# Kernel optimization log

Measured on AMD Instinct MI355X. Metric: run time of the kernel, lower is better.

## Reference

```python
import jax, jax.numpy as jnp
import numpy as np

LN2 = float(np.log(2.0))
N_ATOMS = 100_000
N_PAIRS = 2_000_000
F = 64     # number_of_atom_features
R = 16     # number_of_radial_basis_functions
N_RES = 3


def setup_inputs() -> dict:
    key = jax.random.key(0)
    ks = jax.random.split(key, 16)
    s = 0.05
    inp = {
        "pair_indices": jax.random.randint(ks[0], (2, N_PAIRS), 0, N_ATOMS, dtype=jnp.int32),
        "f_ij": jax.random.normal(ks[1], (N_PAIRS, 1, R), dtype=jnp.float32),
        "d_ij": jax.random.uniform(ks[2], (N_PAIRS, 1), dtype=jnp.float32),
        "atomic_embedding": jax.random.normal(ks[3], (N_ATOMS, F), dtype=jnp.float32),
        # AttentionMask parameter G: [F, R]
        "G": jax.random.normal(ks[4], (F, R), dtype=jnp.float32),
        # interaction_i / interaction_j linear layers (stored as [in, out])
        "Wi": jax.random.normal(ks[5], (F, F), dtype=jnp.float32) * s,
        "bi": jnp.zeros((F,), dtype=jnp.float32),
        "Wj": jax.random.normal(ks[6], (F, F), dtype=jnp.float32) * s,
        "bj": jnp.zeros((F,), dtype=jnp.float32),
        # residual blocks, stacked over N_RES
        "res_W1": jax.random.normal(ks[7], (N_RES, F, F), dtype=jnp.float32) * s,
        "res_b1": jnp.zeros((N_RES, F), dtype=jnp.float32),
        "res_W2": jax.random.normal(ks[8], (N_RES, F, F), dtype=jnp.float32) * s,
        "res_b2": jnp.zeros((N_RES, F), dtype=jnp.float32),
        # process_v linear
        "Wv": jax.random.normal(ks[9], (F, F), dtype=jnp.float32) * s,
        "bv": jnp.zeros((F,), dtype=jnp.float32),
    }
    return inp


def reference(pair_indices, f_ij, d_ij, atomic_embedding,
              G, Wi, bi, Wj, bj, res_W1, res_b1, res_W2, res_b2, Wv, bv):
    idx_i, idx_j = pair_indices[0], pair_indices[1]
    f = f_ij.squeeze(1)                                  # [P, R]

    # ShiftedSoftplus on node embeddings
    x = jax.nn.softplus(atomic_embedding) - LN2          # [N, F]

    x_i_prime = jax.nn.softplus(x @ Wi + bi)             # [N, F]
    x_j_prime = jax.nn.softplus(x[idx_j] @ Wj + bj)      # [P, F] (gather)
    f_prime = f @ G.T                                    # [P, F] attention mask

    msg = x_j_prime * f_prime                            # [P, F]
    summed = jax.ops.segment_sum(msg, idx_i, num_segments=atomic_embedding.shape[0])

    v = x_i_prime + summed                               # [N, F]
    for l in range(res_W1.shape[0]):
        h = jax.nn.softplus(v @ res_W1[l] + res_b1[l])
        v = v + (h @ res_W2[l] + res_b2[l])
    return jax.nn.softplus(v) @ Wv + bv
```

## Files before the change

### kernel.cpp

```cpp
#include <hip/hip_runtime.h>
#include <math.h>

#define FDIM 64
#define RDIM 16
#define LN2F 0.69314718055994530942f
#define LTS 68
#define NBINR 14336
#define NCHUNK 64

typedef __bf16 bf8_t __attribute__((ext_vector_type(8)));
typedef float  f4_t  __attribute__((ext_vector_type(4)));
typedef _Float16 h2_t __attribute__((ext_vector_type(2)));

__device__ __forceinline__ float sp(float x) {
    return fmaxf(x, 0.0f) + __logf(1.0f + __expf(-fabsf(x)));
}

__device__ __forceinline__ float fdot2f(h2_t a, h2_t b, float c) {
#if __has_builtin(__builtin_amdgcn_fdot2)
    return __builtin_amdgcn_fdot2(a, b, c, false);
#else
    return c + (float)a[0] * (float)b[0] + (float)a[1] * (float)b[1];
#endif
}

__device__ __forceinline__ void cvt_store16(_Float16* dst, float4 A, float4 B,
                                            float4 C4, float4 D)
{
    h2_t hv[8];
    hv[0] = h2_t{(_Float16)A.x,  (_Float16)A.y};
    hv[1] = h2_t{(_Float16)A.z,  (_Float16)A.w};
    hv[2] = h2_t{(_Float16)B.x,  (_Float16)B.y};
    hv[3] = h2_t{(_Float16)B.z,  (_Float16)B.w};
    hv[4] = h2_t{(_Float16)C4.x, (_Float16)C4.y};
    hv[5] = h2_t{(_Float16)C4.z, (_Float16)C4.w};
    hv[6] = h2_t{(_Float16)D.x,  (_Float16)D.y};
    hv[7] = h2_t{(_Float16)D.z,  (_Float16)D.w};
    *(uint4*)dst       = *(const uint4*)&hv[0];
    *(uint4*)(dst + 8) = *(const uint4*)&hv[4];
}

__global__ __launch_bounds__(256) void k_prep(
    const float* s0, const float* s1, const float* s2, const float* s3,
    const float* s4, const float* s5, const float* s6, const float* s7,
    const float* s8, __bf16* __restrict__ dst)
{
    const float* srcs[9] = {s0, s1, s2, s3, s4, s5, s6, s7, s8};
    const float* W = srcs[blockIdx.x];
    __bf16* d = dst + (size_t)blockIdx.x * 4096;
    for (int slot = threadIdx.x; slot < 512; slot += 256) {
        int f = slot >> 6, l = slot & 63;
        int kt = f >> 2, nt = f & 3;
        int row0 = kt * 32 + (l >> 4) * 8;
        int col = nt * 16 + (l & 15);
#pragma unroll
        for (int j = 0; j < 8; ++j)
            d[slot * 8 + j] = (__bf16)W[(row0 + j) * FDIM + col];
    }
}

__global__ __launch_bounds__(256) void k_hist2(
    const int* __restrict__ idx_i, int* __restrict__ Cmat,
    int P, int N, int nRange)
{
    __shared__ int h[NBINR];
    const int chunk = blockIdx.x / nRange;
    const int range = blockIdx.x % nRange;
    const int lo = range * NBINR;
    const int nb = min(NBINR, N - lo);
    for (int u = threadIdx.x; u < NBINR; u += 256) h[u] = 0;
    __syncthreads();

    const int chunkSz = (P + NCHUNK - 1) / NCHUNK;
    const int cs = chunk * chunkSz;
    const int ce = min(P, cs + chunkSz);
    int p = cs + threadIdx.x;
    for (; p + 768 < ce; p += 1024) {
        int i0 = idx_i[p];
        int i1 = idx_i[p + 256];
        int i2 = idx_i[p + 512];
        int i3 = idx_i[p + 768];
        unsigned u0 = (unsigned)(i0 - lo);
        unsigned u1 = (unsigned)(i1 - lo);
        unsigned u2 = (unsigned)(i2 - lo);
        unsigned u3 = (unsigned)(i3 - lo);
        if (u0 < (unsigned)nb) atomicAdd(&h[u0], 1);
        if (u1 < (unsigned)nb) atomicAdd(&h[u1], 1);
        if (u2 < (unsigned)nb) atomicAdd(&h[u2], 1);
        if (u3 < (unsigned)nb) atomicAdd(&h[u3], 1);
    }
    for (; p < ce; p += 256) {
        unsigned u = (unsigned)(idx_i[p] - lo);
        if (u < (unsigned)nb) atomicAdd(&h[u], 1);
    }
    __syncthreads();
    for (int u = threadIdx.x; u < nb; u += 256)
        Cmat[(size_t)chunk * N + lo + u] = h[u];
}

__global__ __launch_bounds__(256) void k_scanR(
    int* __restrict__ Cmat, int* __restrict__ tot, int N)
{
    const int bA = blockIdx.x * 512 + threadIdx.x;
    const int bB = bA + 256;
    const bool okA = bA < N, okB = bB < N;
    int runA = 0, runB = 0;
    for (int c = 0; c < NCHUNK; ++c) {
        const size_t base = (size_t)c * N;
        if (okA) { int val = Cmat[base + bA]; Cmat[base + bA] = runA; runA += val; }
        if (okB) { int val = Cmat[base + bB]; Cmat[base + bB] = runB; runB += val; }
    }
    if (okA) tot[bA] = runA;
    if (okB) tot[bB] = runB;
}

__device__ __forceinline__ void tile_in(float* T, const float* __restrict__ src,
                                        int a0, int rows, int lane)
{
#pragma unroll 4
    for (int i = 0; i < 16; ++i) {
        int r = i * 4 + (lane >> 4);
        int col = (lane & 15) * 4;
        float4 val = make_float4(0.f, 0.f, 0.f, 0.f);
        if (r < rows) val = *(const float4*)&src[(size_t)(a0 + r) * FDIM + col];
        *(float4*)&T[r * LTS + col] = val;
    }
}

__device__ __forceinline__ void build_a(const float* T, int lane, bool actLn2,
                                        bf8_t (&aF)[4][2])
{
    const int l15 = lane & 15, quad = lane >> 4;
#pragma unroll
    for (int mt = 0; mt < 4; ++mt) {
#pragma unroll
        for (int kt = 0; kt < 2; ++kt) {
            const float* rp = &T[(mt * 16 + l15) * LTS + kt * 32 + quad * 8];
            float4 u0 = *(const float4*)rp;
            float4 u1 = *(const float4*)(rp + 4);
            float e[8] = {u0.x, u0.y, u0.z, u0.w, u1.x, u1.y, u1.z, u1.w};
            bf8_t f;
#pragma unroll
            for (int j = 0; j < 8; ++j) {
                float t = actLn2 ? (sp(e[j]) - LN2F) : e[j];
                f[j] = (__bf16)t;
            }
            aF[mt][kt] = f;
        }
    }
}

__global__ __launch_bounds__(256) void k_atoms(
    const float* __restrict__ emb, const __bf16* __restrict__ wf,
    const float* __restrict__ bi, const float* __restrict__ bj,
    float* __restrict__ v, _Float16* __restrict__ y16, int N)
{
    __shared__ float tile[4][64 * LTS];
    const int lane = threadIdx.x & 63;
    const int wv = threadIdx.x >> 6;
    float* T = tile[wv];
    const int l15 = lane & 15, quad = lane >> 4;

    const bf8_t* wiF = (const bf8_t*)wf;
    const bf8_t* wjF = (const bf8_t*)(wf + 4096);
    bf8_t wi[2][4], wj[2][4];
#pragma unroll
    for (int kt = 0; kt < 2; ++kt)
#pragma unroll
        for (int nt = 0; nt < 4; ++nt) {
            wi[kt][nt] = wiF[(kt * 4 + nt) * 64 + lane];
            wj[kt][nt] = wjF[(kt * 4 + nt) * 64 + lane];
        }
    float biv[4], bjv[4];
#pragma unroll
    for (int nt = 0; nt < 4; ++nt) {
        biv[nt] = bi[nt * 16 + l15];
        bjv[nt] = bj[nt * 16 + l15];
    }

    const int nTiles = (N + 63) >> 6;
    for (int t = blockIdx.x * 4 + wv; t < nTiles; t += gridDim.x * 4) {
        const int a0 = t << 6;
        const int rows = min(64, N - a0);
        tile_in(T, emb, a0, rows, lane);
        bf8_t aF[4][2];
        build_a(T, lane, true, aF);
#pragma unroll
        for (int mt = 0; mt < 4; ++mt)
#pragma unroll
            for (int nt = 0; nt < 4; ++nt) {
                f4_t acc = {biv[nt], biv[nt], biv[nt], biv[nt]};
                acc = __builtin_amdgcn_mfma_f32_16x16x32_bf16(aF[mt][0], wi[0][nt], acc, 0, 0, 0);
                acc = __builtin_amdgcn_mfma_f32_16x16x32_bf16(aF[mt][1], wi[1][nt], acc, 0, 0, 0);
#pragma unroll
                for (int reg = 0; reg < 4; ++reg) {
                    int r = mt * 16 + quad * 4 + reg;
                    if (r < rows) v[(size_t)(a0 + r) * FDIM + nt * 16 + l15] = sp(acc[reg]);
                }
            }
#pragma unroll
        for (int mt = 0; mt < 4; ++mt)
#pragma unroll
            for (int nt = 0; nt < 4; ++nt) {
                f4_t acc = {bjv[nt], bjv[nt], bjv[nt], bjv[nt]};
                acc = __builtin_amdgcn_mfma_f32_16x16x32_bf16(aF[mt][0], wj[0][nt], acc, 0, 0, 0);
                acc = __builtin_amdgcn_mfma_f32_16x16x32_bf16(aF[mt][1], wj[1][nt], acc, 0, 0, 0);
#pragma unroll
                for (int reg = 0; reg < 4; ++reg) {
                    int r = mt * 16 + quad * 4 + reg;
                    if (r < rows)
                        y16[(size_t)(a0 + r) * FDIM + nt * 16 + l15] = (_Float16)sp(acc[reg]);
                }
            }
    }
}

__global__ __launch_bounds__(256) void k_post(
    const __bf16* __restrict__ wf,
    const float* __restrict__ rb1, const float* __restrict__ rb2,
    const float* __restrict__ bv,
    float* __restrict__ v, int N)
{
    __shared__ float tile[4][64 * LTS];
    const int lane = threadIdx.x & 63;
    const int wv = threadIdx.x >> 6;
    float* T = tile[wv];
    const int l15 = lane & 15, quad = lane >> 4;

    float b1v[3][4], b2v[3][4], bvv[4];
#pragma unroll
    for (int l = 0; l < 3; ++l)
#pragma unroll
        for (int nt = 0; nt < 4; ++nt) {
            b1v[l][nt] = rb1[l * FDIM + nt * 16 + l15];
            b2v[l][nt] = rb2[l * FDIM + nt * 16 + l15];
        }
#pragma unroll
    for (int nt = 0; nt < 4; ++nt) bvv[nt] = bv[nt * 16 + l15];

    const int nTiles = (N + 63) >> 6;
    for (int t = blockIdx.x * 4 + wv; t < nTiles; t += gridDim.x * 4) {
        const int a0 = t << 6;
        const int rows = min(64, N - a0);
        tile_in(T, v, a0, rows, lane);
        float vC[16][4];
#pragma unroll
        for (int mt = 0; mt < 4; ++mt)
#pragma unroll
            for (int nt = 0; nt < 4; ++nt)
#pragma unroll
                for (int reg = 0; reg < 4; ++reg)
                    vC[mt * 4 + nt][reg] =
                        T[(mt * 16 + quad * 4 + reg) * LTS + nt * 16 + l15];

        for (int l = 0; l < 3; ++l) {
            const bf8_t* w1f = (const bf8_t*)(wf + (size_t)(2 * l) * 4096);
            const bf8_t* w2f = (const bf8_t*)(wf + (size_t)(2 * l + 1) * 4096);
            bf8_t aF[4][2];
            build_a(T, lane, false, aF);
#pragma unroll
            for (int mt = 0; mt < 4; ++mt)
#pragma unroll
                for (int nt = 0; nt < 4; ++nt) {
                    f4_t acc = {b1v[l][nt], b1v[l][nt], b1v[l][nt], b1v[l][nt]};
                    acc = __builtin_amdgcn_mfma_f32_16x16x32_bf16(aF[mt][0], w1f[(0 * 4 + nt) * 64 + lane], acc, 0, 0, 0);
                    acc = __builtin_amdgcn_mfma_f32_16x16x32_bf16(aF[mt][1], w1f[(1 * 4 + nt) * 64 + lane], acc, 0, 0, 0);
#pragma unroll
                    for (int reg = 0; reg < 4; ++reg)
                        T[(mt * 16 + quad * 4 + reg) * LTS + nt * 16 + l15] = sp(acc[reg]);
                }
            bf8_t hF[4][2];
            build_a(T, lane, false, hF);
#pragma unroll
            for (int mt = 0; mt < 4; ++mt)
#pragma unroll
                for (int nt = 0; nt < 4; ++nt) {
                    f4_t acc = {b2v[l][nt], b2v[l][nt], b2v[l][nt], b2v[l][nt]};
                    acc = __builtin_amdgcn_mfma_f32_16x16x32_bf16(hF[mt][0], w2f[(0 * 4 + nt) * 64 + lane], acc, 0, 0, 0);
                    acc = __builtin_amdgcn_mfma_f32_16x16x32_bf16(hF[mt][1], w2f[(1 * 4 + nt) * 64 + lane], acc, 0, 0, 0);
#pragma unroll
                    for (int reg = 0; reg < 4; ++reg)
                        vC[mt * 4 + nt][reg] += acc[reg];
                }
            if (l < 2) {
#pragma unroll
                for (int mt = 0; mt < 4; ++mt)
#pragma unroll
                    for (int nt = 0; nt < 4; ++nt)
#pragma unroll
                        for (int reg = 0; reg < 4; ++reg)
                            T[(mt * 16 + quad * 4 + reg) * LTS + nt * 16 + l15] =
                                vC[mt * 4 + nt][reg];
            }
        }
#pragma unroll
        for (int mt = 0; mt < 4; ++mt)
#pragma unroll
            for (int nt = 0; nt < 4; ++nt)
#pragma unroll
                for (int reg = 0; reg < 4; ++reg)
                    T[(mt * 16 + quad * 4 + reg) * LTS + nt * 16 + l15] =
                        sp(vC[mt * 4 + nt][reg]);
        bf8_t fF[4][2];
        build_a(T, lane, false, fF);
        const bf8_t* wvf = (const bf8_t*)(wf + (size_t)6 * 4096);
#pragma unroll
        for (int mt = 0; mt < 4; ++mt)
#pragma unroll
            for (int nt = 0; nt < 4; ++nt) {
                f4_t acc = {bvv[nt], bvv[nt], bvv[nt], bvv[nt]};
                acc = __builtin_amdgcn_mfma_f32_16x16x32_bf16(fF[mt][0], wvf[(0 * 4 + nt) * 64 + lane], acc, 0, 0, 0);
                acc = __builtin_amdgcn_mfma_f32_16x16x32_bf16(fF[mt][1], wvf[(1 * 4 + nt) * 64 + lane], acc, 0, 0, 0);
#pragma unroll
                for (int reg = 0; reg < 4; ++reg) {
                    int r = mt * 16 + quad * 4 + reg;
                    if (r < rows) v[(size_t)(a0 + r) * FDIM + nt * 16 + l15] = acc[reg];
                }
            }
    }
}

__global__ __launch_bounds__(256) void k_scan_a(
    const int* __restrict__ cnt, int* __restrict__ part, int N)
{
    __shared__ int red[256];
    int b = blockIdx.x, t = threadIdx.x;
    int base = b * 1024 + t * 4;
    int s = 0;
#pragma unroll
    for (int i = 0; i < 4; ++i) { int a = base + i; if (a < N) s += cnt[a]; }
    red[t] = s; __syncthreads();
    for (int off = 128; off > 0; off >>= 1) {
        if (t < off) red[t] += red[t + off];
        __syncthreads();
    }
    if (t == 0) part[b] = red[0];
}

__global__ __launch_bounds__(256) void k_scan_b(int* __restrict__ part, int nPart)
{
    __shared__ int lds[256];
    int t = threadIdx.x;
    int base = t * 4;
    int v[4]; int s = 0;
#pragma unroll
    for (int i = 0; i < 4; ++i) { v[i] = (base + i < nPart) ? part[base + i] : 0; s += v[i]; }
    lds[t] = s; __syncthreads();
    int run = s;
    for (int off = 1; off < 256; off <<= 1) {
        int x = (t >= off) ? lds[t - off] : 0;
        __syncthreads();
        lds[t] += x;
        __syncthreads();
    }
    int excl = lds[t] - run;
#pragma unroll
    for (int i = 0; i < 4; ++i) { if (base + i < nPart) { part[base + i] = excl; excl += v[i]; } }
}

__global__ __launch_bounds__(256) void k_scan_c(
    const int* __restrict__ cnt, const int* __restrict__ part,
    int* __restrict__ start, int N, int P)
{
    __shared__ int lds[256];
    int b = blockIdx.x, t = threadIdx.x;
    int base = b * 1024 + t * 4;
    int v[4]; int s = 0;
#pragma unroll
    for (int i = 0; i < 4; ++i) { int a = base + i; v[i] = (a < N) ? cnt[a] : 0; s += v[i]; }
    lds[t] = s; __syncthreads();
    int run = s;
    for (int off = 1; off < 256; off <<= 1) {
        int x = (t >= off) ? lds[t - off] : 0;
        __syncthreads();
        lds[t] += x;
        __syncthreads();
    }
    int pre = part[b] + (lds[t] - run);
#pragma unroll
    for (int i = 0; i < 4; ++i) {
        int a = base + i;
        if (a < N) { start[a] = pre; pre += v[i]; }
    }
    if (b == 0 && t == 0) start[N] = P;
}

__global__ __launch_bounds__(256) void k_scatter2(
    const int* __restrict__ pidx, const int* __restrict__ Cmat,
    const int* __restrict__ start, int* __restrict__ sortedJ,
    int* __restrict__ invPos, int P, int N, int nRange)
{
    __shared__ int cur[NBINR];
    const int chunk = blockIdx.x / nRange;
    const int range = blockIdx.x % nRange;
    const int lo = range * NBINR;
    const int nb = min(NBINR, N - lo);
    for (int u = threadIdx.x; u < nb; u += 256)
        cur[u] = start[lo + u] + Cmat[(size_t)chunk * N + lo + u];
    __syncthreads();

    const int chunkSz = (P + NCHUNK - 1) / NCHUNK;
    const int cs = chunk * chunkSz;
    const int ce = min(P, cs + chunkSz);
    int p = cs + threadIdx.x;
    for (; p + 768 < ce; p += 1024) {
        int i0 = pidx[p];
        int i1 = pidx[p + 256];
        int i2 = pidx[p + 512];
        int i3 = pidx[p + 768];
        int j0 = pidx[P + p];
        int j1 = pidx[P + p + 256];
        int j2 = pidx[P + p + 512];
        int j3 = pidx[P + p + 768];
        unsigned u0 = (unsigned)(i0 - lo);
        unsigned u1 = (unsigned)(i1 - lo);
        unsigned u2 = (unsigned)(i2 - lo);
        unsigned u3 = (unsigned)(i3 - lo);
        if (u0 < (unsigned)nb) { int pos = atomicAdd(&cur[u0], 1); sortedJ[pos] = j0; invPos[p] = pos; }
        if (u1 < (unsigned)nb) { int pos = atomicAdd(&cur[u1], 1); sortedJ[pos] = j1; invPos[p + 256] = pos; }
        if (u2 < (unsigned)nb) { int pos = atomicAdd(&cur[u2], 1); sortedJ[pos] = j2; invPos[p + 512] = pos; }
        if (u3 < (unsigned)nb) { int pos = atomicAdd(&cur[u3], 1); sortedJ[pos] = j3; invPos[p + 768] = pos; }
    }
    for (; p < ce; p += 256) {
        int i = pidx[p];
        unsigned u = (unsigned)(i - lo);
        if (u < (unsigned)nb) {
            int j = pidx[P + p];
            int pos = atomicAdd(&cur[u], 1);
            sortedJ[pos] = j;
            invPos[p] = pos;
        }
    }
}

__global__ __launch_bounds__(256) void k_gatherF2(
    const float* __restrict__ f_ij, const int* __restrict__ invPos,
    _Float16* __restrict__ sortedF, int P)
{
    int t = blockIdx.x * blockDim.x + threadIdx.x;
    int n = gridDim.x * blockDim.x;
    int p = t;
    for (; p + 3 * n < P; p += 4 * n) {
        int q0 = invPos[p];
        int q1 = invPos[p + n];
        int q2 = invPos[p + 2 * n];
        int q3 = invPos[p + 3 * n];
        const float4* f0 = (const float4*)(f_ij + (size_t)p * RDIM);
        const float4* f1 = (const float4*)(f_ij + (size_t)(p + n) * RDIM);
        const float4* f2 = (const float4*)(f_ij + (size_t)(p + 2 * n) * RDIM);
        const float4* f3 = (const float4*)(f_ij + (size_t)(p + 3 * n) * RDIM);
        float4 a0 = f0[0], b0 = f0[1], c0 = f0[2], d0 = f0[3];
        float4 a1 = f1[0], b1 = f1[1], c1 = f1[2], d1 = f1[3];
        float4 a2 = f2[0], b2 = f2[1], c2 = f2[2], d2 = f2[3];
        float4 a3 = f3[0], b3 = f3[1], c3 = f3[2], d3 = f3[3];
        cvt_store16(sortedF + (size_t)q0 * 16, a0, b0, c0, d0);
        cvt_store16(sortedF + (size_t)q1 * 16, a1, b1, c1, d1);
        cvt_store16(sortedF + (size_t)q2 * 16, a2, b2, c2, d2);
        cvt_store16(sortedF + (size_t)q3 * 16, a3, b3, c3, d3);
    }
    for (; p < P; p += n) {
        int q = invPos[p];
        const float4* fp = (const float4*)(f_ij + (size_t)p * RDIM);
        float4 A = fp[0], B = fp[1], C4 = fp[2], D = fp[3];
        cvt_store16(sortedF + (size_t)q * 16, A, B, C4, D);
    }
}

__global__ __launch_bounds__(256) void k_seg(
    const int* __restrict__ sortedJ, const _Float16* __restrict__ sortedF,
    const int* __restrict__ start, const float* __restrict__ G,
    const _Float16* __restrict__ y16, float* __restrict__ v, int N)
{
    const int c = threadIdx.x & 63;
    const int w = __builtin_amdgcn_readfirstlane((blockIdx.x << 2) | (threadIdx.x >> 6));
    const int nw = gridDim.x << 2;

    h2_t g2[8];
    {
        const float4* gp = (const float4*)(G + c * RDIM);
        float4 g0 = gp[0], g1 = gp[1], g2v = gp[2], g3 = gp[3];
        g2[0] = h2_t{(_Float16)g0.x, (_Float16)g0.y};
        g2[1] = h2_t{(_Float16)g0.z, (_Float16)g0.w};
        g2[2] = h2_t{(_Float16)g1.x, (_Float16)g1.y};
        g2[3] = h2_t{(_Float16)g1.z, (_Float16)g1.w};
        g2[4] = h2_t{(_Float16)g2v.x, (_Float16)g2v.y};
        g2[5] = h2_t{(_Float16)g2v.z, (_Float16)g2v.w};
        g2[6] = h2_t{(_Float16)g3.x, (_Float16)g3.y};
        g2[7] = h2_t{(_Float16)g3.z, (_Float16)g3.w};
    }

    for (int a = w; a < N; a += nw) {
        const int s = __builtin_amdgcn_readfirstlane(start[a]);
        const int e = __builtin_amdgcn_readfirstlane(start[a + 1]);
        float vold = v[(size_t)a * FDIM + c];
        float acc0 = 0.f, acc1 = 0.f, acc2 = 0.f, acc3 = 0.f;

        for (int base = s; base < e; base += 64) {
            const int nn = (e - base < 64) ? (e - base) : 64;
            const int li = (c < nn) ? c : (nn - 1);
            const int jkv = sortedJ[base + li];

            int k = 0;
            for (; k + 8 <= nn; k += 8) {
                int jj[8];
#pragma unroll
                for (int u = 0; u < 8; ++u)
                    jj[u] = __builtin_amdgcn_readlane(jkv, k + u);
                float yv[8];
#pragma unroll
                for (int u = 0; u < 8; ++u)
                    yv[u] = (float)y16[(size_t)jj[u] * FDIM + c];
                const h2_t* f2 = (const h2_t*)(sortedF + (size_t)(base + k) * 16);
#pragma unroll
                for (int u = 0; u < 8; ++u) {
                    float d = 0.f;
#pragma unroll
                    for (int r = 0; r < 8; ++r)
                        d = fdot2f(f2[u * 8 + r], g2[r], d);
                    if ((u & 3) == 0) acc0 = fmaf(d, yv[u], acc0);
                    else if ((u & 3) == 1) acc1 = fmaf(d, yv[u], acc1);
                    else if ((u & 3) == 2) acc2 = fmaf(d, yv[u], acc2);
                    else acc3 = fmaf(d, yv[u], acc3);
                }
            }
            for (; k < nn; ++k) {
                const int j0 = __builtin_amdgcn_readlane(jkv, k);
                float y0 = (float)y16[(size_t)j0 * FDIM + c];
                const h2_t* f2 = (const h2_t*)(sortedF + (size_t)(base + k) * 16);
                float d = 0.f;
#pragma unroll
                for (int r = 0; r < 8; ++r)
                    d = fdot2f(f2[r], g2[r], d);
                acc0 = fmaf(d, y0, acc0);
            }
        }

        v[(size_t)a * FDIM + c] = vold + (acc0 + acc1) + (acc2 + acc3);
    }
}

extern "C" void kernel_launch(void* const* d_in, const int* in_sizes, int n_in,
                              void* d_out, int out_size, void* d_ws, size_t ws_size,
                              hipStream_t stream)
{
    const int*   pidx = (const int*)d_in[0];
    const float* f_ij = (const float*)d_in[1];
    const float* emb  = (const float*)d_in[3];
    const float* G    = (const float*)d_in[4];
    const float* Wi   = (const float*)d_in[5];
    const float* bi   = (const float*)d_in[6];
    const float* Wj   = (const float*)d_in[7];
    const float* bj   = (const float*)d_in[8];
    const float* rW1  = (const float*)d_in[9];
    const float* rb1  = (const float*)d_in[10];
    const float* rW2  = (const float*)d_in[11];
    const float* rb2  = (const float*)d_in[12];
    const float* Wv   = (const float*)d_in[13];
    const float* bv   = (const float*)d_in[14];

    const int P = in_sizes[0] / 2;
    const int N = in_sizes[3] / FDIM;

    float* v = (float*)d_out;

    char* ws = (char*)d_ws;
    size_t off = 0;
    _Float16* y16  = (_Float16*)(ws + off);
    int*    Cmat   = (int*)(ws + off);    off += (size_t)N * FDIM * 4;
    int*    tot    = (int*)(ws + off);    off += (size_t)N * 4;
    int*    start  = (int*)(ws + off);    off += (size_t)(N + 1) * 4;
    off = (off + 15) & ~(size_t)15;
    int*    part   = (int*)(ws + off);    off += (size_t)4096 * 4;
    off = (off + 15) & ~(size_t)15;
    int*    sortedJ = (int*)(ws + off);   off += (size_t)P * 4;
    off = (off + 15) & ~(size_t)15;
    int*    invPos  = (int*)(ws + off);   off += (size_t)P * 4;
    off = (off + 63) & ~(size_t)63;
    _Float16* sortedF = (_Float16*)(ws + off); off += (size_t)P * 16 * 2;
    off = (off + 15) & ~(size_t)15;
    __bf16* wf     = (__bf16*)(ws + off); off += (size_t)9 * 4096 * 2;

    const int nRange = (N + NBINR - 1) / NBINR;
    const int nPart = (N + 1023) / 1024;
    const int nTiles = (N + 63) >> 6;
    const int gTiles = (nTiles + 3) / 4;

    dim3 blk(256);
    k_prep<<<9, blk, 0, stream>>>(Wi, Wj, rW1, rW2, rW1 + 4096, rW2 + 4096,
                                  rW1 + 8192, rW2 + 8192, Wv, wf);
    k_hist2<<<NCHUNK * nRange, blk, 0, stream>>>(pidx, Cmat, P, N, nRange);
    k_scanR<<<(N + 511) / 512, blk, 0, stream>>>(Cmat, tot, N);
    k_scan_a<<<nPart, blk, 0, stream>>>(tot, part, N);
    k_scan_b<<<1, blk, 0, stream>>>(part, nPart);
    k_scan_c<<<nPart, blk, 0, stream>>>(tot, part, start, N, P);
    k_scatter2<<<NCHUNK * nRange, blk, 0, stream>>>(pidx, Cmat, start, sortedJ,
                                                    invPos, P, N, nRange);
    k_gatherF2<<<2048, blk, 0, stream>>>(f_ij, invPos, sortedF, P);
    k_atoms<<<gTiles, blk, 0, stream>>>(emb, wf, bi, bj, v, y16, N);
    k_seg<<<4096, blk, 0, stream>>>(sortedJ, sortedF, start, G, y16, v, N);
    k_post<<<gTiles, blk, 0, stream>>>(wf + (size_t)2 * 4096, rb1, rb2, bv, v, N);
}
```

Baseline: 640.6 us.

## Replace sorted f_ij scatter with in-order fp16 copy and indirect reads

Instead of permuting f_ij into sorted order through an invPos scatter kernel, f_ij is converted to fp16 in original order and the scatter records (pair index, j) pairs. The segment kernel then reads each pair's 32-byte radial row indirectly by original pair index. This removes the random-write gather pass and the invPos array, but the segment kernel's f reads become random 32-byte loads instead of contiguous ones, and each wave does extra readlanes.

```diff
diff --git a/kernel.cpp b/kernel.cpp
--- a/kernel.cpp
+++ b/kernel.cpp
@@ -38,6 +38,18 @@
     hv[7] = h2_t{(_Float16)D.z,  (_Float16)D.w};
     *(uint4*)dst       = *(const uint4*)&hv[0];
     *(uint4*)(dst + 8) = *(const uint4*)&hv[4];
+}
+
+__global__ __launch_bounds__(256) void k_cvtF(
+    const float* __restrict__ f_ij, _Float16* __restrict__ f16, int P)
+{
+    int t = blockIdx.x * blockDim.x + threadIdx.x;
+    int n = gridDim.x * blockDim.x;
+    for (int p = t; p < P; p += n) {
+        const float4* fp = (const float4*)(f_ij + (size_t)p * RDIM);
+        float4 A = fp[0], B = fp[1], C4 = fp[2], D = fp[3];
+        cvt_store16(f16 + (size_t)p * RDIM, A, B, C4, D);
+    }
 }
 
 __global__ __launch_bounds__(256) void k_prep(
@@ -387,8 +399,8 @@
 
 __global__ __launch_bounds__(256) void k_scatter2(
     const int* __restrict__ pidx, const int* __restrict__ Cmat,
-    const int* __restrict__ start, int* __restrict__ sortedJ,
-    int* __restrict__ invPos, int P, int N, int nRange)
+    const int* __restrict__ start, int2* __restrict__ sorted,
+    int P, int N, int nRange)
 {
     __shared__ int cur[NBINR];
     const int chunk = blockIdx.x / nRange;
@@ -416,10 +428,10 @@
         unsigned u1 = (unsigned)(i1 - lo);
         unsigned u2 = (unsigned)(i2 - lo);
         unsigned u3 = (unsigned)(i3 - lo);
-        if (u0 < (unsigned)nb) { int pos = atomicAdd(&cur[u0], 1); sortedJ[pos] = j0; invPos[p] = pos; }
-        if (u1 < (unsigned)nb) { int pos = atomicAdd(&cur[u1], 1); sortedJ[pos] = j1; invPos[p + 256] = pos; }
-        if (u2 < (unsigned)nb) { int pos = atomicAdd(&cur[u2], 1); sortedJ[pos] = j2; invPos[p + 512] = pos; }
-        if (u3 < (unsigned)nb) { int pos = atomicAdd(&cur[u3], 1); sortedJ[pos] = j3; invPos[p + 768] = pos; }
+        if (u0 < (unsigned)nb) { int pos = atomicAdd(&cur[u0], 1); sorted[pos] = make_int2(p, j0); }
+        if (u1 < (unsigned)nb) { int pos = atomicAdd(&cur[u1], 1); sorted[pos] = make_int2(p + 256, j1); }
+        if (u2 < (unsigned)nb) { int pos = atomicAdd(&cur[u2], 1); sorted[pos] = make_int2(p + 512, j2); }
+        if (u3 < (unsigned)nb) { int pos = atomicAdd(&cur[u3], 1); sorted[pos] = make_int2(p + 768, j3); }
     }
     for (; p < ce; p += 256) {
         int i = pidx[p];
@@ -427,47 +439,13 @@
         if (u < (unsigned)nb) {
             int j = pidx[P + p];
             int pos = atomicAdd(&cur[u], 1);
-            sortedJ[pos] = j;
-            invPos[p] = pos;
+            sorted[pos] = make_int2(p, j);
         }
     }
 }
 
-__global__ __launch_bounds__(256) void k_gatherF2(
-    const float* __restrict__ f_ij, const int* __restrict__ invPos,
-    _Float16* __restrict__ sortedF, int P)
-{
-    int t = blockIdx.x * blockDim.x + threadIdx.x;
-    int n = gridDim.x * blockDim.x;
-    int p = t;
-    for (; p + 3 * n < P; p += 4 * n) {
-        int q0 = invPos[p];
-        int q1 = invPos[p + n];
-        int q2 = invPos[p + 2 * n];
-        int q3 = invPos[p + 3 * n];
-        const float4* f0 = (const float4*)(f_ij + (size_t)p * RDIM);
-        const float4* f1 = (const float4*)(f_ij + (size_t)(p + n) * RDIM);
-        const float4* f2 = (const float4*)(f_ij + (size_t)(p + 2 * n) * RDIM);
-        const float4* f3 = (const float4*)(f_ij + (size_t)(p + 3 * n) * RDIM);
-        float4 a0 = f0[0], b0 = f0[1], c0 = f0[2], d0 = f0[3];
-        float4 a1 = f1[0], b1 = f1[1], c1 = f1[2], d1 = f1[3];
-        float4 a2 = f2[0], b2 = f2[1], c2 = f2[2], d2 = f2[3];
-        float4 a3 = f3[0], b3 = f3[1], c3 = f3[2], d3 = f3[3];
-        cvt_store16(sortedF + (size_t)q0 * 16, a0, b0, c0, d0);
-        cvt_store16(sortedF + (size_t)q1 * 16, a1, b1, c1, d1);
-        cvt_store16(sortedF + (size_t)q2 * 16, a2, b2, c2, d2);
-        cvt_store16(sortedF + (size_t)q3 * 16, a3, b3, c3, d3);
-    }
-    for (; p < P; p += n) {
-        int q = invPos[p];
-        const float4* fp = (const float4*)(f_ij + (size_t)p * RDIM);
-        float4 A = fp[0], B = fp[1], C4 = fp[2], D = fp[3];
-        cvt_store16(sortedF + (size_t)q * 16, A, B, C4, D);
-    }
-}
-
 __global__ __launch_bounds__(256) void k_seg(
-    const int* __restrict__ sortedJ, const _Float16* __restrict__ sortedF,
+    const int2* __restrict__ sorted, const _Float16* __restrict__ f16,
     const int* __restrict__ start, const float* __restrict__ G,
     const _Float16* __restrict__ y16, float* __restrict__ v, int N)
 {
@@ -498,25 +476,28 @@
         for (int base = s; base < e; base += 64) {
             const int nn = (e - base < 64) ? (e - base) : 64;
             const int li = (c < nn) ? c : (nn - 1);
-            const int jkv = sortedJ[base + li];
+            const int2 E = sorted[base + li];
+            const int pk = E.x, jk = E.y;
 
             int k = 0;
             for (; k + 8 <= nn; k += 8) {
-                int jj[8];
-#pragma unroll
-                for (int u = 0; u < 8; ++u)
-                    jj[u] = __builtin_amdgcn_readlane(jkv, k + u);
+                int pp[8], jj[8];
+#pragma unroll
+                for (int u = 0; u < 8; ++u) {
+                    pp[u] = __builtin_amdgcn_readlane(pk, k + u);
+                    jj[u] = __builtin_amdgcn_readlane(jk, k + u);
+                }
                 float yv[8];
 #pragma unroll
                 for (int u = 0; u < 8; ++u)
                     yv[u] = (float)y16[(size_t)jj[u] * FDIM + c];
-                const h2_t* f2 = (const h2_t*)(sortedF + (size_t)(base + k) * 16);
 #pragma unroll
                 for (int u = 0; u < 8; ++u) {
+                    const h2_t* fr = (const h2_t*)(f16 + (size_t)pp[u] * RDIM);
                     float d = 0.f;
 #pragma unroll
                     for (int r = 0; r < 8; ++r)
-                        d = fdot2f(f2[u * 8 + r], g2[r], d);
+                        d = fdot2f(fr[r], g2[r], d);
                     if ((u & 3) == 0) acc0 = fmaf(d, yv[u], acc0);
                     else if ((u & 3) == 1) acc1 = fmaf(d, yv[u], acc1);
                     else if ((u & 3) == 2) acc2 = fmaf(d, yv[u], acc2);
@@ -524,13 +505,14 @@
                 }
             }
             for (; k < nn; ++k) {
-                const int j0 = __builtin_amdgcn_readlane(jkv, k);
+                const int p0 = __builtin_amdgcn_readlane(pk, k);
+                const int j0 = __builtin_amdgcn_readlane(jk, k);
                 float y0 = (float)y16[(size_t)j0 * FDIM + c];
-                const h2_t* f2 = (const h2_t*)(sortedF + (size_t)(base + k) * 16);
+                const h2_t* fr = (const h2_t*)(f16 + (size_t)p0 * RDIM);
                 float d = 0.f;
 #pragma unroll
                 for (int r = 0; r < 8; ++r)
-                    d = fdot2f(f2[r], g2[r], d);
+                    d = fdot2f(fr[r], g2[r], d);
                 acc0 = fmaf(d, y0, acc0);
             }
         }
@@ -572,11 +554,9 @@
     off = (off + 15) & ~(size_t)15;
     int*    part   = (int*)(ws + off);    off += (size_t)4096 * 4;
     off = (off + 15) & ~(size_t)15;
-    int*    sortedJ = (int*)(ws + off);   off += (size_t)P * 4;
-    off = (off + 15) & ~(size_t)15;
-    int*    invPos  = (int*)(ws + off);   off += (size_t)P * 4;
+    int2*   sorted = (int2*)(ws + off);   off += (size_t)P * 8;
     off = (off + 63) & ~(size_t)63;
-    _Float16* sortedF = (_Float16*)(ws + off); off += (size_t)P * 16 * 2;
+    _Float16* f16  = (_Float16*)(ws + off); off += (size_t)P * RDIM * 2;
     off = (off + 15) & ~(size_t)15;
     __bf16* wf     = (__bf16*)(ws + off); off += (size_t)9 * 4096 * 2;
 
@@ -588,15 +568,14 @@
     dim3 blk(256);
     k_prep<<<9, blk, 0, stream>>>(Wi, Wj, rW1, rW2, rW1 + 4096, rW2 + 4096,
                                   rW1 + 8192, rW2 + 8192, Wv, wf);
+    k_cvtF<<<2048, blk, 0, stream>>>(f_ij, f16, P);
     k_hist2<<<NCHUNK * nRange, blk, 0, stream>>>(pidx, Cmat, P, N, nRange);
     k_scanR<<<(N + 511) / 512, blk, 0, stream>>>(Cmat, tot, N);
     k_scan_a<<<nPart, blk, 0, stream>>>(tot, part, N);
     k_scan_b<<<1, blk, 0, stream>>>(part, nPart);
     k_scan_c<<<nPart, blk, 0, stream>>>(tot, part, start, N, P);
-    k_scatter2<<<NCHUNK * nRange, blk, 0, stream>>>(pidx, Cmat, start, sortedJ,
-                                                    invPos, P, N, nRange);
-    k_gatherF2<<<2048, blk, 0, stream>>>(f_ij, invPos, sortedF, P);
+    k_scatter2<<<NCHUNK * nRange, blk, 0, stream>>>(pidx, Cmat, start, sorted, P, N, nRange);
     k_atoms<<<gTiles, blk, 0, stream>>>(emb, wf, bi, bj, v, y16, N);
-    k_seg<<<4096, blk, 0, stream>>>(sortedJ, sortedF, start, G, y16, v, N);
+    k_seg<<<4096, blk, 0, stream>>>(sorted, f16, start, G, y16, v, N);
     k_post<<<gTiles, blk, 0, stream>>>(wf + (size_t)2 * 4096, rb1, rb2, bv, v, N);
 }
```

After: 609.3 us. -4.9%, faster.
